# Performance work log

Measured on AMD Instinct MI355X. Metric: run time of the kernel, lower is better.

Reference implementation:

```python
import jax, jax.numpy as jnp
import numpy as np


def setup_inputs() -> dict:
    key = jax.random.key(0)
    k1, k2 = jax.random.split(key)
    query = jax.random.normal(k1, (16, 256, 32, 32), dtype=jnp.float32)
    search_map = jax.random.normal(k2, (16, 256, 64, 64), dtype=jnp.float32)
    return {"query": query, "search_map": search_map}


def reference(query, search_map):
    # query: [bs, c, h, w]; search_map: [bs, c, H, W]
    bs, c, h, w = query.shape
    # pad H and W by h//2, w//2 on each side (matches F.pad(left,right,top,bottom))
    padded = jnp.pad(search_map, ((0, 0), (0, 0), (h // 2, h // 2), (w // 2, w // 2)))

    def corr_one(map_, q_):
        # map_: [c, Hp, Wp], q_: [c, h, w]
        # per-sample cross-correlation: the query acts as a single-output conv kernel
        out = jax.lax.conv_general_dilated(
            map_[None],            # [1, c, Hp, Wp]
            q_[None],              # [1, c, h, w] -> OIHW
            window_strides=(1, 1),
            padding="VALID",
            dimension_numbers=("NCHW", "OIHW", "NCHW"),
        )
        return out[0]              # [1, Hout, Wout]

    # vmap over the batch: each sample uses its own query as the kernel
    return jax.vmap(corr_one)(padded, query)  # [bs, 1, Hout, Wout]
```

## Files before the change

### kernel.cpp

```cpp
#include <hip/hip_runtime.h>
#include <stdint.h>

typedef __bf16 bf16x8 __attribute__((ext_vector_type(8)));
typedef float  f32x4  __attribute__((ext_vector_type(4)));
typedef uint32_t u32x4 __attribute__((ext_vector_type(4)));

__device__ __forceinline__ uint16_t f2bf(float f) {
    uint32_t u = __builtin_bit_cast(uint32_t, f);
    u += 0x7FFFu + ((u >> 16) & 1u);
    return (uint16_t)(u >> 16);
}

__global__ __launch_bounds__(256) void qtrans_kernel(const float* __restrict__ Q,
                                                     uint16_t* __restrict__ Qt,
                                                     float* __restrict__ out) {
    __shared__ float T[8 * 1064];
    const int ch = blockIdx.x, b = blockIdx.y;
    const int tid = threadIdx.x;

    {
        int g = (b * 32 + ch) * 256 + tid;
        if (g < 67600) out[g] = 0.f;
    }

    const float* src = Q + ((size_t)(b * 256 + ch * 8)) * 1024;
    #pragma unroll
    for (int it = 0; it < 32; ++it) {
        int r = tid + it * 256;
        int c8 = r >> 10, rem = r & 1023;
        T[c8 * 1064 + (rem >> 5) * 33 + (rem & 31)] = src[(size_t)c8 * 1024 + rem];
    }
    __syncthreads();

    uint32_t* dst = (uint32_t*)Qt;
    #pragma unroll
    for (int it = 0; it < 16; ++it) {
        int o2 = tid + it * 256;
        int t  = (o2 & 3) * 2;
        int il = (o2 >> 2) & 15;
        int j  = (o2 >> 6) & 31;
        int ih = (o2 >> 11) & 1;
        float v0 = T[t * 1064 + (ih * 16 + il) * 33 + j];
        float v1 = T[(t + 1) * 1064 + (ih * 16 + il) * 33 + j];
        uint32_t pk = (uint32_t)f2bf(v0) | ((uint32_t)f2bf(v1) << 16);
        size_t oi = ((((size_t)(b * 2 + ih) * 32 + j) * 32 + ch) * 16 + il) * 4 + (t >> 1);
        dst[oi] = pk;
    }
}

__global__ __launch_bounds__(256, 4) void corr_kernel(const float* __restrict__ S,
                                                      const uint16_t* __restrict__ Qt,
                                                      float* __restrict__ out) {
    __shared__ __align__(16) char smem[40960];
    uint16_t* S_l = (uint16_t*)smem;
    float*    Pw  = (float*)smem;

    const int bid = blockIdx.x;
    const int b = bid & 15, d = bid >> 4;
    const int tid = threadIdx.x, wave = tid >> 6, lane = tid & 63;
    const int l15 = lane & 15, l4 = lane >> 4;

    {
        const u32x4 z = {};
        for (int zi = tid; zi < 512; zi += 256) {
            int ch = zi >> 4, r = zi & 15;
            *(u32x4*)&S_l[ch * 640 + r * 8] = z;
        }
    }
    {
        const int sx = tid & 63, w = tid >> 6;
        const float* sp = S + ((size_t)b * 256) * 4096 + (size_t)d * 64;
        #pragma unroll
        for (int k = 0; k < 8; ++k) {
            int ch = w * 8 + k;
            float v[8];
            #pragma unroll
            for (int cc = 0; cc < 8; ++cc)
                v[cc] = sp[(size_t)(ch * 8 + cc) * 4096 + sx];
            u32x4 pk;
            #pragma unroll
            for (int q = 0; q < 4; ++q)
                pk[q] = (uint32_t)f2bf(v[2 * q]) | ((uint32_t)f2bf(v[2 * q + 1]) << 16);
            *(u32x4*)&S_l[ch * 640 + (sx + 16) * 8] = pk;
        }
    }

    const uint16_t* Bb = Qt + (size_t)b * 262144 + l4 * 128 + l15 * 8;

    bf16x8 C0, C1, C2, C3;
    {
        const int s0 = (2 * wave) & 7;
        const uint16_t* p0 = Bb + wave * 4096 + s0 * 512;
        C0 = *(const bf16x8*)(p0);
        C1 = *(const bf16x8*)(p0 + 131072);
        C2 = *(const bf16x8*)(p0 + 65536);
        C3 = *(const bf16x8*)(p0 + 196608);
    }

    __syncthreads();

    f32x4 acc[5][2] = {};

    #pragma unroll
    for (int n = 0; n < 32; ++n) {
        const int jj = n >> 3;
        const int s  = ((n & 7) + 2 * wave) & 7;
        const int j0a = wave + jj * 4;

        const int nn = (n < 31) ? (n + 1) : 31;
        const int jn = nn >> 3;
        const int sn = ((nn & 7) + 2 * wave) & 7;
        const uint16_t* pn = Bb + (wave + jn * 4) * 4096 + sn * 512;
        bf16x8 N0 = *(const bf16x8*)(pn);
        bf16x8 N1 = *(const bf16x8*)(pn + 131072);
        bf16x8 N2 = *(const bf16x8*)(pn + 65536);
        bf16x8 N3 = *(const bf16x8*)(pn + 196608);
        __builtin_amdgcn_sched_barrier(0);

        const int chb = (s * 4 + l4) * 640;
        bf16x8 A[5];
        #pragma unroll
        for (int t = 0; t < 5; ++t) {
            int rr = j0a + t * 16 + l15;
            rr = (rr < 80) ? rr : 0;
            A[t] = *(const bf16x8*)&S_l[chb + rr * 8];
        }

        #pragma unroll
        for (int t = 0; t < 5; ++t) {
            acc[t][0] = __builtin_amdgcn_mfma_f32_16x16x32_bf16(A[t], C0, acc[t][0], 0, 0, 0);
            acc[t][1] = __builtin_amdgcn_mfma_f32_16x16x32_bf16(A[t], C1, acc[t][1], 0, 0, 0);
        }
        #pragma unroll
        for (int t = 1; t < 5; ++t) {
            acc[t - 1][0] = __builtin_amdgcn_mfma_f32_16x16x32_bf16(A[t], C2, acc[t - 1][0], 0, 0, 0);
            acc[t - 1][1] = __builtin_amdgcn_mfma_f32_16x16x32_bf16(A[t], C3, acc[t - 1][1], 0, 0, 0);
        }

        C0 = N0; C1 = N1; C2 = N2; C3 = N3;
    }

    __syncthreads();
    {
        float* pw = Pw + wave * 2560;
        #pragma unroll
        for (int m = 0; m < 5; ++m)
            #pragma unroll
            for (int n = 0; n < 2; ++n)
                *(f32x4*)&pw[(n * 16 + l15) * 80 + m * 16 + l4 * 4] = acc[m][n];
    }
    __syncthreads();
    for (int e = tid; e < 65 * 32; e += 256) {
        int x = e % 65, i = e / 65;
        int y = d - i + 16;
        if ((unsigned)y < 65u) {
            float v = Pw[0 * 2560 + i * 80 + x] + Pw[1 * 2560 + i * 80 + x]
                    + Pw[2 * 2560 + i * 80 + x] + Pw[3 * 2560 + i * 80 + x];
            atomicAdd(out + ((size_t)b * 4225 + (size_t)y * 65 + x), v);
        }
    }
}

__global__ __launch_bounds__(256) void naive_kernel(const float* __restrict__ Q,
                                                    const float* __restrict__ S,
                                                    float* __restrict__ out) {
    int gid = blockIdx.x * 256 + threadIdx.x;
    if (gid >= 67600) return;
    int b = gid / 4225, r = gid % 4225, y = r / 65, x = r % 65;
    int jlo = 16 - x; if (jlo < 0) jlo = 0;
    int jhi = 80 - x; if (jhi > 32) jhi = 32;
    float acc = 0.f;
    for (int c = 0; c < 256; ++c) {
        const float* Sb = S + ((size_t)(b * 256 + c)) * 4096;
        const float* Qb = Q + ((size_t)(b * 256 + c)) * 1024;
        for (int i = 0; i < 32; ++i) {
            int dd = y + i - 16;
            if ((unsigned)dd >= 64u) continue;
            const float* Sr = Sb + dd * 64 + (x - 16);
            const float* Qr = Qb + i * 32;
            for (int j = jlo; j < jhi; ++j) acc += Sr[j] * Qr[j];
        }
    }
    out[gid] = acc;
}

extern "C" void kernel_launch(void* const* d_in, const int* in_sizes, int n_in,
                              void* d_out, int out_size, void* d_ws, size_t ws_size,
                              hipStream_t stream) {
    (void)in_sizes; (void)n_in; (void)out_size;
    const float* Q = (const float*)d_in[0];
    const float* S = (const float*)d_in[1];
    float* out = (float*)d_out;

    const size_t QT_BYTES = (size_t)16 * 2 * 32 * 32 * 16 * 8 * 2;

    if (ws_size < QT_BYTES) {
        naive_kernel<<<(67600 + 255) / 256, 256, 0, stream>>>(Q, S, out);
        return;
    }
    uint16_t* Qt = (uint16_t*)d_ws;

    qtrans_kernel<<<dim3(32, 16), 256, 0, stream>>>(Q, Qt, out);
    corr_kernel<<<1024, 256, 0, stream>>>(S, Qt, out);
}
```

Measured before the change: 132.7 us.

## Overlap second-half search-map staging with MFMA compute of first half

The kernel now loads and converts only the first 128 channels of the search map into LDS before the compute loop. It streams the remaining 128 channels from global memory into LDS during the first 16 MFMA iterations, with a barrier at iteration 16 before they are read. The iteration order over channel slices changes to match. This is meant to hide global-load latency behind matrix work, at the cost of extra registers and a mid-loop barrier.

```diff
diff --git a/kernel.cpp b/kernel.cpp
--- a/kernel.cpp
+++ b/kernel.cpp
@@ -59,6 +59,7 @@
     const int b = bid & 15, d = bid >> 4;
     const int tid = threadIdx.x, wave = tid >> 6, lane = tid & 63;
     const int l15 = lane & 15, l4 = lane >> 4;
+    const int sx = lane;
 
     {
         const u32x4 z = {};
@@ -67,30 +68,28 @@
             *(u32x4*)&S_l[ch * 640 + r * 8] = z;
         }
     }
-    {
-        const int sx = tid & 63, w = tid >> 6;
-        const float* sp = S + ((size_t)b * 256) * 4096 + (size_t)d * 64;
-        #pragma unroll
-        for (int k = 0; k < 8; ++k) {
-            int ch = w * 8 + k;
-            float v[8];
-            #pragma unroll
-            for (int cc = 0; cc < 8; ++cc)
-                v[cc] = sp[(size_t)(ch * 8 + cc) * 4096 + sx];
-            u32x4 pk;
-            #pragma unroll
-            for (int q = 0; q < 4; ++q)
-                pk[q] = (uint32_t)f2bf(v[2 * q]) | ((uint32_t)f2bf(v[2 * q + 1]) << 16);
-            *(u32x4*)&S_l[ch * 640 + (sx + 16) * 8] = pk;
-        }
+
+    const float* sp = S + ((size_t)b * 256) * 4096 + (size_t)d * 64;
+
+    #pragma unroll
+    for (int k = 0; k < 4; ++k) {
+        const int ch = k * 4 + wave;
+        float v[8];
+        #pragma unroll
+        for (int cc = 0; cc < 8; ++cc)
+            v[cc] = sp[(size_t)(ch * 8 + cc) * 4096 + sx];
+        u32x4 pk;
+        #pragma unroll
+        for (int q = 0; q < 4; ++q)
+            pk[q] = (uint32_t)f2bf(v[2 * q]) | ((uint32_t)f2bf(v[2 * q + 1]) << 16);
+        *(u32x4*)&S_l[ch * 640 + (sx + 16) * 8] = pk;
     }
 
     const uint16_t* Bb = Qt + (size_t)b * 262144 + l4 * 128 + l15 * 8;
 
     bf16x8 C0, C1, C2, C3;
     {
-        const int s0 = (2 * wave) & 7;
-        const uint16_t* p0 = Bb + wave * 4096 + s0 * 512;
+        const uint16_t* p0 = Bb + wave * 4096 + wave * 512;
         C0 = *(const bf16x8*)(p0);
         C1 = *(const bf16x8*)(p0 + 131072);
         C2 = *(const bf16x8*)(p0 + 65536);
@@ -100,22 +99,41 @@
     __syncthreads();
 
     f32x4 acc[5][2] = {};
+    float vs[8];
 
     #pragma unroll
     for (int n = 0; n < 32; ++n) {
-        const int jj = n >> 3;
-        const int s  = ((n & 7) + 2 * wave) & 7;
+        if (n == 16) __syncthreads();
+
+        const int h  = n >> 4;
+        const int jj = (n & 15) >> 2;
+        const int s  = h * 4 + (((n & 3) + wave) & 3);
         const int j0a = wave + jj * 4;
 
         const int nn = (n < 31) ? (n + 1) : 31;
-        const int jn = nn >> 3;
-        const int sn = ((nn & 7) + 2 * wave) & 7;
+        const int hn = nn >> 4;
+        const int jn = (nn & 15) >> 2;
+        const int sn = hn * 4 + (((nn & 3) + wave) & 3);
         const uint16_t* pn = Bb + (wave + jn * 4) * 4096 + sn * 512;
         bf16x8 N0 = *(const bf16x8*)(pn);
         bf16x8 N1 = *(const bf16x8*)(pn + 131072);
         bf16x8 N2 = *(const bf16x8*)(pn + 65536);
         bf16x8 N3 = *(const bf16x8*)(pn + 196608);
-        __builtin_amdgcn_sched_barrier(0);
+
+        if (n == 0 || n == 4 || n == 8 || n == 12) {
+            const int ch = (n >> 2) * 4 + wave;
+            #pragma unroll
+            for (int cc = 0; cc < 8; ++cc)
+                vs[cc] = sp[(size_t)(128 + ch * 8 + cc) * 4096 + sx];
+        }
+        if (n == 2 || n == 6 || n == 10 || n == 14) {
+            const int ch = ((n - 2) >> 2) * 4 + wave;
+            u32x4 pk;
+            #pragma unroll
+            for (int q = 0; q < 4; ++q)
+                pk[q] = (uint32_t)f2bf(vs[2 * q]) | ((uint32_t)f2bf(vs[2 * q + 1]) << 16);
+            *(u32x4*)&S_l[(16 + ch) * 640 + (sx + 16) * 8] = pk;
+        }
 
         const int chb = (s * 4 + l4) * 640;
         bf16x8 A[5];
@@ -125,6 +143,7 @@
             rr = (rr < 80) ? rr : 0;
             A[t] = *(const bf16x8*)&S_l[chb + rr * 8];
         }
+        __builtin_amdgcn_sched_barrier(0);
 
         #pragma unroll
         for (int t = 0; t < 5; ++t) {
```

After: 166.9 us. +25.7%, slower.
